# Kernel tuning notes

Hardware: AMD Instinct MI355X
Metric: run time of the kernel (lower is better)

Reference implementation:

```python
import jax, jax.numpy as jnp
import numpy as np

D_MODEL = 1024
N_HEAD = 16
DEPTH = D_MODEL // N_HEAD
NEG = -10000.0


def setup_inputs() -> dict:
    key = jax.random.key(0)
    ks = jax.random.split(key, 10)
    B, N = 4, 2048
    s = 1.0 / np.sqrt(D_MODEL)
    inp = {
        "input": jax.random.normal(ks[0], (B, N, D_MODEL), dtype=jnp.float32),
        "mask": jnp.tril(jnp.ones((N, N), dtype=bool)),  # causal; True = attend
        "Wq": jax.random.normal(ks[1], (D_MODEL, D_MODEL), dtype=jnp.float32) * s,
        "bq": jnp.zeros((D_MODEL,), dtype=jnp.float32),
        "Wk": jax.random.normal(ks[2], (D_MODEL, D_MODEL), dtype=jnp.float32) * s,
        "bk": jnp.zeros((D_MODEL,), dtype=jnp.float32),
        "Wv": jax.random.normal(ks[3], (D_MODEL, D_MODEL), dtype=jnp.float32) * s,
        "bv": jnp.zeros((D_MODEL,), dtype=jnp.float32),
        "Wo": jax.random.normal(ks[4], (D_MODEL, D_MODEL), dtype=jnp.float32) * s,
        "bo": jnp.zeros((D_MODEL,), dtype=jnp.float32),
    }
    return inp


def reference(input, mask, Wq, bq, Wk, bk, Wv, bv, Wo, bo):
    b, n, _ = input.shape
    # torch Linear: x @ W.T + b  (dropout is identity in eval)
    q = (input @ Wq.T + bq).reshape(b, n, N_HEAD, DEPTH)
    k = (input @ Wk.T + bk).reshape(b, n, N_HEAD, DEPTH)
    v = (input @ Wv.T + bv).reshape(b, n, N_HEAD, DEPTH)
    # per-head scale is sqrt(depth) (ScaledDotProductAttention built with d_model=depth)
    scale = jnp.sqrt(jnp.asarray(DEPTH, dtype=input.dtype))
    scores = jnp.einsum("bnhd,bmhd->bhnm", q, k) / scale
    scores = jnp.where(mask, scores, NEG)
    attn = jax.nn.softmax(scores, axis=-1)
    out = jnp.einsum("bhnm,bmhd->bnhd", attn, v).reshape(b, n, D_MODEL)
    return out @ Wo.T + bo
```

## Files before the change

### kernel.cpp

```cpp
#include <hip/hip_runtime.h>
#include <hip/hip_bf16.h>
#include <stdint.h>

#define D_MODEL 1024
#define N_HEAD  16
#define DEPTH   64
#define BATCH   4
#define SEQ     2048
#define ROWS    (BATCH*SEQ)
#define LOG2E   1.4426950408889634f
#define QSCALE  0.18033688292839513f

typedef unsigned short u16;
typedef __attribute__((ext_vector_type(8))) short short8;
typedef __attribute__((ext_vector_type(4))) float f32x4;

__device__ inline u16 f2bf(float f) {
  union { float f; unsigned u; } v; v.f = f;
  unsigned r = v.u + 0x7FFFu + ((v.u >> 16) & 1u);
  return (u16)(r >> 16);
}

__device__ inline unsigned cvt_pk_bf16(float lo, float hi) {
  unsigned w;
  asm("v_cvt_pk_bf16_f32 %0, %1, %2" : "=v"(w) : "v"(lo), "v"(hi));
  return w;
}

__device__ inline void gll16(const void* g, void* l) {
  __builtin_amdgcn_global_load_lds(
      (const __attribute__((address_space(1))) void*)g,
      (__attribute__((address_space(3))) void*)l, 16, 0, 0);
}

__global__ __launch_bounds__(256) void cvt_all(
    const float4* __restrict__ X,  const float4* __restrict__ Wq,
    const float4* __restrict__ Wk, const float4* __restrict__ Wv,
    const float4* __restrict__ Wo,
    u16* __restrict__ Xb, u16* __restrict__ Wqkvb, u16* __restrict__ Wob)
{
  const int b = blockIdx.x;
  const float4* src; u16* dst; int lb;
  if      (b < 8192)  { src = X;  dst = Xb;                        lb = b; }
  else if (b < 9216)  { src = Wq; dst = Wqkvb;                     lb = b - 8192; }
  else if (b < 10240) { src = Wk; dst = Wqkvb + D_MODEL*D_MODEL;   lb = b - 9216; }
  else if (b < 11264) { src = Wv; dst = Wqkvb + 2*D_MODEL*D_MODEL; lb = b - 10240; }
  else                { src = Wo; dst = Wob;                       lb = b - 11264; }
  const int i = lb*256 + threadIdx.x;
  float4 v = src[i];
  ushort4 o;
  o.x = f2bf(v.x); o.y = f2bf(v.y); o.z = f2bf(v.z); o.w = f2bf(v.w);
  *(ushort4*)(dst + 4*(size_t)i) = o;
}

__global__ __launch_bounds__(256) void gemm_qkv(
    const u16* __restrict__ A, const u16* __restrict__ Bm,
    const float* __restrict__ bq, const float* __restrict__ bk,
    const float* __restrict__ bvp,
    u16* __restrict__ Qo, u16* __restrict__ Ko, u16* __restrict__ Vo)
{
  constexpr int K = D_MODEL, BK = 64;
  __shared__ __align__(16) u16 As[128*BK];
  __shared__ __align__(16) u16 Bs[128*BK];
  const int tid = threadIdx.x;
  const int wave = tid >> 6, lane = tid & 63;
  const int g = lane >> 4, c = lane & 15;
  const int m0 = blockIdx.x * 128, n0 = blockIdx.y * 128;
  const int wr = (wave >> 1) * 64, wc = (wave & 1) * 64;
  f32x4 acc[4][4] = {};

  int aRow[4], aCol[4];
#pragma unroll
  for (int cc = 0; cc < 4; ++cc) {
    int L = (wave*4 + cc)*1024 + lane*16;
    int U = L ^ (((L >> 7) & 7) << 4);
    aRow[cc] = U >> 7;
    aCol[cc] = (U & 127) >> 1;
  }

  for (int k0 = 0; k0 < K; k0 += BK) {
#pragma unroll
    for (int cc = 0; cc < 4; ++cc) {
      int chunk = wave*4 + cc;
      gll16(A  + (size_t)(m0 + aRow[cc])*K + k0 + aCol[cc], (char*)As + chunk*1024);
      gll16(Bm + (size_t)(n0 + aRow[cc])*K + k0 + aCol[cc], (char*)Bs + chunk*1024);
    }
    __syncthreads();
#pragma unroll
    for (int ks = 0; ks < 2; ++ks) {
      short8 af[4], bf[4];
#pragma unroll
      for (int rb = 0; rb < 4; ++rb) {
        int row = wr + rb*16 + c;
        int addr = (row*128 + ks*64 + g*16) ^ ((row & 7) << 4);
        af[rb] = *(const short8*)((const char*)As + addr);
      }
#pragma unroll
      for (int cb = 0; cb < 4; ++cb) {
        int row = wc + cb*16 + c;
        int addr = (row*128 + ks*64 + g*16) ^ ((row & 7) << 4);
        bf[cb] = *(const short8*)((const char*)Bs + addr);
      }
#pragma unroll
      for (int rb = 0; rb < 4; ++rb)
#pragma unroll
        for (int cb = 0; cb < 4; ++cb)
          acc[rb][cb] = __builtin_amdgcn_mfma_f32_16x16x32_bf16(af[rb], bf[cb], acc[rb][cb], 0, 0, 0);
    }
    __syncthreads();
  }

  const int mode = n0 >> 10;
  const float* bias = (mode == 0) ? bq : (mode == 1) ? bk : bvp;

#pragma unroll
  for (int rb = 0; rb < 4; ++rb) {
#pragma unroll
    for (int cb = 0; cb < 4; ++cb) {
      int colg = n0 + wc + cb*16 + c;
      int cl = colg & 1023;
      int h = cl >> 6, d = cl & 63;
      float bv = bias[cl];
      if (mode == 2) {
        int rg = m0 + wr + rb*16 + g*4;
        int b = rg >> 11, n = rg & 2047;
        ushort4 o;
        o.x = f2bf(acc[rb][cb][0] + bv);
        o.y = f2bf(acc[rb][cb][1] + bv);
        o.z = f2bf(acc[rb][cb][2] + bv);
        o.w = f2bf(acc[rb][cb][3] + bv);
        *(ushort4*)&Vo[(((size_t)(b*N_HEAD + h))*DEPTH + d)*SEQ + n] = o;
      } else {
        u16* dst = (mode == 0) ? Qo : Ko;
        float sc = (mode == 0) ? QSCALE : 1.0f;
#pragma unroll
        for (int r = 0; r < 4; ++r) {
          int rowg = m0 + wr + rb*16 + g*4 + r;
          int b = rowg >> 11, n = rowg & 2047;
          dst[(((size_t)(b*N_HEAD + h))*SEQ + n)*DEPTH + d] = f2bf((acc[rb][cb][r] + bv) * sc);
        }
      }
    }
  }
}

__global__ __launch_bounds__(256) void gemm_out(
    const u16* __restrict__ A, const u16* __restrict__ Bm,
    const float* __restrict__ bias, float* __restrict__ Cout,
    int M, int N, int K)
{
  constexpr int BK = 64;
  __shared__ __align__(16) u16 As[128*BK];
  __shared__ __align__(16) u16 Bs[128*BK];
  const int tid = threadIdx.x;
  const int wave = tid >> 6, lane = tid & 63;
  const int g = lane >> 4, c = lane & 15;
  const int m0 = blockIdx.x * 128, n0 = blockIdx.y * 128;
  const int wr = (wave >> 1) * 64, wc = (wave & 1) * 64;
  f32x4 acc[4][4] = {};

  int aRow[4], aCol[4];
#pragma unroll
  for (int cc = 0; cc < 4; ++cc) {
    int L = (wave*4 + cc)*1024 + lane*16;
    int U = L ^ (((L >> 7) & 7) << 4);
    aRow[cc] = U >> 7;
    aCol[cc] = (U & 127) >> 1;
  }

  for (int k0 = 0; k0 < K; k0 += BK) {
#pragma unroll
    for (int cc = 0; cc < 4; ++cc) {
      int chunk = wave*4 + cc;
      gll16(A  + (size_t)(m0 + aRow[cc])*K + k0 + aCol[cc], (char*)As + chunk*1024);
      gll16(Bm + (size_t)(n0 + aRow[cc])*K + k0 + aCol[cc], (char*)Bs + chunk*1024);
    }
    __syncthreads();
#pragma unroll
    for (int ks = 0; ks < 2; ++ks) {
      short8 af[4], bf[4];
#pragma unroll
      for (int rb = 0; rb < 4; ++rb) {
        int row = wr + rb*16 + c;
        int addr = (row*128 + ks*64 + g*16) ^ ((row & 7) << 4);
        af[rb] = *(const short8*)((const char*)As + addr);
      }
#pragma unroll
      for (int cb = 0; cb < 4; ++cb) {
        int row = wc + cb*16 + c;
        int addr = (row*128 + ks*64 + g*16) ^ ((row & 7) << 4);
        bf[cb] = *(const short8*)((const char*)Bs + addr);
      }
#pragma unroll
      for (int rb = 0; rb < 4; ++rb)
#pragma unroll
        for (int cb = 0; cb < 4; ++cb)
          acc[rb][cb] = __builtin_amdgcn_mfma_f32_16x16x32_bf16(af[rb], bf[cb], acc[rb][cb], 0, 0, 0);
    }
    __syncthreads();
  }

#pragma unroll
  for (int rb = 0; rb < 4; ++rb) {
#pragma unroll
    for (int cb = 0; cb < 4; ++cb) {
      int colg = n0 + wc + cb*16 + c;
      float bv = bias[colg];
#pragma unroll
      for (int r = 0; r < 4; ++r) {
        int rowg = m0 + wr + rb*16 + g*4 + r;
        Cout[(size_t)rowg * N + colg] = acc[rb][cb][r] + bv;
      }
    }
  }
}

__global__ __launch_bounds__(512) void flash(
    const u16* __restrict__ Q, const u16* __restrict__ K,
    const u16* __restrict__ VT, u16* __restrict__ O)
{
  __shared__ __align__(16) u16 Ks[2][64*64];
  __shared__ __align__(16) u16 Vs[2][64*64];
  const int tid = threadIdx.x, wave = tid >> 6, lane = tid & 63;
  const int g = lane >> 4, c = lane & 15;
  const int bh = blockIdx.y, b = bh >> 4, h = bh & 15;
  const int qt = gridDim.x - 1 - blockIdx.x;
  const int q0 = qt * 128;
  const int qg = q0 + wave*16 + c;
  const u16* Qh = Q  + (size_t)bh * SEQ * DEPTH;
  const u16* Kh = K  + (size_t)bh * SEQ * DEPTH;
  const u16* Vh = VT + (size_t)bh * DEPTH * SEQ;

  short8 qf[2];
#pragma unroll
  for (int ks = 0; ks < 2; ++ks)
    qf[ks] = *(const short8*)(Qh + (size_t)(q0 + wave*16 + c)*DEPTH + ks*32 + g*8);

  f32x4 o[4] = {};
  float m_r = -3.0e38f, l_r = 0.0f;

  const int src1 = (c + (((2*g)  & 3) << 4)) << 2;
  const int src2 = (c + (((2*g+1)& 3) << 4)) << 2;
  const bool hi = (g >> 1) & 1;

  int sRow, sCol;
  {
    int L = wave*1024 + lane*16;
    int U = L ^ (((L >> 7) & 7) << 4);
    sRow = U >> 7; sCol = (U & 127) >> 1;
  }

  auto stage = [&](int t, int bsel) {
    const int kv0 = t * 64;
    gll16(Kh + (size_t)(kv0 + sRow)*DEPTH + sCol, (char*)Ks[bsel] + wave*1024);
    gll16(Vh + (size_t)sRow*SEQ + kv0 + sCol,     (char*)Vs[bsel] + wave*1024);
  };

  const int ntiles = 2*qt + 2;
  stage(0, 0);
  __syncthreads();
  int cur = 0;

  for (int t = 0; t < ntiles; ++t) {
    if (t + 1 < ntiles) stage(t + 1, cur ^ 1);
    const int kv0 = t * 64;

    if (kv0 <= q0 + wave*16 + 15) {
      const char* Kc = (const char*)Ks[cur];
      const char* Vc = (const char*)Vs[cur];

      f32x4 s[4] = {};
#pragma unroll
      for (int ks = 0; ks < 2; ++ks)
#pragma unroll
        for (int cb = 0; cb < 4; ++cb) {
          int row = cb*16 + c;
          int addr = (row*128 + ks*64 + g*16) ^ ((row & 7) << 4);
          short8 kf = *(const short8*)(Kc + addr);
          s[cb] = __builtin_amdgcn_mfma_f32_16x16x32_bf16(kf, qf[ks], s[cb], 0, 0, 0);
        }

      if (t >= ntiles - 2) {
#pragma unroll
        for (int cb = 0; cb < 4; ++cb)
#pragma unroll
          for (int r = 0; r < 4; ++r)
            if (kv0 + cb*16 + g*4 + r > qg) s[cb][r] = -3.0e38f;
      }

      float mx = s[0][0];
#pragma unroll
      for (int cb = 0; cb < 4; ++cb)
#pragma unroll
        for (int r = 0; r < 4; ++r) mx = fmaxf(mx, s[cb][r]);
      mx = fmaxf(mx, __shfl_xor(mx, 16));
      mx = fmaxf(mx, __shfl_xor(mx, 32));

      float mn = fmaxf(m_r, mx);
      float alpha = exp2f(m_r - mn);
      m_r = mn;

      float sum = 0.f;
      unsigned pk01[4], pk23[4];
#pragma unroll
      for (int cb = 0; cb < 4; ++cb) {
        float p0 = exp2f(s[cb][0] - mn);
        float p1 = exp2f(s[cb][1] - mn);
        float p2 = exp2f(s[cb][2] - mn);
        float p3 = exp2f(s[cb][3] - mn);
        sum += (p0 + p1) + (p2 + p3);
        pk01[cb] = cvt_pk_bf16(p0, p1);
        pk23[cb] = cvt_pk_bf16(p2, p3);
      }
      sum += __shfl_xor(sum, 16);
      sum += __shfl_xor(sum, 32);
      l_r = l_r*alpha + sum;
#pragma unroll
      for (int db = 0; db < 4; ++db)
#pragma unroll
        for (int r = 0; r < 4; ++r) o[db][r] *= alpha;

#pragma unroll
      for (int js = 0; js < 2; ++js) {
        unsigned a0  = __builtin_amdgcn_ds_bpermute(src1, pk01[2*js]);
        unsigned a0b = __builtin_amdgcn_ds_bpermute(src1, pk01[2*js+1]);
        unsigned a1  = __builtin_amdgcn_ds_bpermute(src1, pk23[2*js]);
        unsigned a1b = __builtin_amdgcn_ds_bpermute(src1, pk23[2*js+1]);
        unsigned b0  = __builtin_amdgcn_ds_bpermute(src2, pk01[2*js]);
        unsigned b0b = __builtin_amdgcn_ds_bpermute(src2, pk01[2*js+1]);
        unsigned b1  = __builtin_amdgcn_ds_bpermute(src2, pk23[2*js]);
        unsigned b1b = __builtin_amdgcn_ds_bpermute(src2, pk23[2*js+1]);
        union { unsigned u[4]; short8 v8; } pf;
        pf.u[0] = hi ? a0b : a0;
        pf.u[1] = hi ? a1b : a1;
        pf.u[2] = hi ? b0b : b0;
        pf.u[3] = hi ? b1b : b1;
#pragma unroll
        for (int db = 0; db < 4; ++db) {
          int row = db*16 + c;
          int addr = (row*128 + js*64 + g*16) ^ ((row & 7) << 4);
          short8 vf = *(const short8*)(Vc + addr);
          o[db] = __builtin_amdgcn_mfma_f32_16x16x32_bf16(vf, pf.v8, o[db], 0, 0, 0);
        }
      }
    }
    __syncthreads();
    cur ^= 1;
  }

  float inv = 1.0f / l_r;
  size_t base = ((size_t)(b*SEQ + qg))*D_MODEL + h*DEPTH;
#pragma unroll
  for (int db = 0; db < 4; ++db) {
    ushort4 w;
    w.x = f2bf(o[db][0] * inv);
    w.y = f2bf(o[db][1] * inv);
    w.z = f2bf(o[db][2] * inv);
    w.w = f2bf(o[db][3] * inv);
    *(ushort4*)&O[base + db*16 + g*4] = w;
  }
}

extern "C" void kernel_launch(void* const* d_in, const int* in_sizes, int n_in,
                              void* d_out, int out_size, void* d_ws, size_t ws_size,
                              hipStream_t stream) {
  const float* X  = (const float*)d_in[0];
  const float* Wq = (const float*)d_in[2];
  const float* bq = (const float*)d_in[3];
  const float* Wk = (const float*)d_in[4];
  const float* bk = (const float*)d_in[5];
  const float* Wv = (const float*)d_in[6];
  const float* bv = (const float*)d_in[7];
  const float* Wo = (const float*)d_in[8];
  const float* bo = (const float*)d_in[9];

  char* w = (char*)d_ws;
  const size_t MB = 1u << 20;
  u16* Xb   = (u16*)(w);
  u16* Qb   = (u16*)(w + 16*MB);
  u16* Kb   = (u16*)(w + 32*MB);
  u16* VTb  = (u16*)(w + 48*MB);
  u16* Ob   = (u16*)(w + 64*MB);
  u16* Wqkv = (u16*)(w + 80*MB);
  u16* Wob  = (u16*)(w + 86*MB);

  cvt_all<<<12288, 256, 0, stream>>>(
      (const float4*)X, (const float4*)Wq, (const float4*)Wk,
      (const float4*)Wv, (const float4*)Wo, Xb, Wqkv, Wob);

  gemm_qkv<<<dim3(ROWS/128, 3*D_MODEL/128), 256, 0, stream>>>(
      Xb, Wqkv, bq, bk, bv, Qb, Kb, VTb);

  flash<<<dim3(SEQ/128, BATCH*N_HEAD), 512, 0, stream>>>(Qb, Kb, VTb, Ob);

  gemm_out<<<dim3(ROWS/128, D_MODEL/128), 256, 0, stream>>>(
      Ob, Wob, bo, (float*)d_out, ROWS, D_MODEL, D_MODEL);
}
```

Measured before the change: 355.6 us.

## Shrink flash query tile to 64 rows with 1D heavy-first grid and setprio

The flash kernel now uses 64-query tiles with 4 waves per block instead of 128-query tiles with 8 waves. It launches a 1D grid of 2048 blocks ordered so the longest causal tiles start first, with each wave staging two chunks of the K/V loads. Every wave in a tile now has live work on every KV tile, so the per-wave causal skip branch is removed and masking happens only on the diagonal tile. s_setprio is raised around the MFMA sections to favour matrix issue. This aims to cut idle waves and improve load balance and occupancy, at the cost of reloading K/V twice as often per query row.

```diff
diff --git a/kernel.cpp b/kernel.cpp
--- a/kernel.cpp
+++ b/kernel.cpp
@@ -215,7 +215,7 @@
   }
 }
 
-__global__ __launch_bounds__(512) void flash(
+__global__ __launch_bounds__(256) void flash(
     const u16* __restrict__ Q, const u16* __restrict__ K,
     const u16* __restrict__ VT, u16* __restrict__ O)
 {
@@ -223,9 +223,10 @@
   __shared__ __align__(16) u16 Vs[2][64*64];
   const int tid = threadIdx.x, wave = tid >> 6, lane = tid & 63;
   const int g = lane >> 4, c = lane & 15;
-  const int bh = blockIdx.y, b = bh >> 4, h = bh & 15;
-  const int qt = gridDim.x - 1 - blockIdx.x;
-  const int q0 = qt * 128;
+  const int bid = blockIdx.x;
+  const int qt = 31 - (bid >> 6);
+  const int bh = bid & 63, b = bh >> 4, h = bh & 15;
+  const int q0 = qt * 64;
   const int qg = q0 + wave*16 + c;
   const u16* Qh = Q  + (size_t)bh * SEQ * DEPTH;
   const u16* Kh = K  + (size_t)bh * SEQ * DEPTH;
@@ -234,7 +235,7 @@
   short8 qf[2];
 #pragma unroll
   for (int ks = 0; ks < 2; ++ks)
-    qf[ks] = *(const short8*)(Qh + (size_t)(q0 + wave*16 + c)*DEPTH + ks*32 + g*8);
+    qf[ks] = *(const short8*)(Qh + (size_t)qg*DEPTH + ks*32 + g*8);
 
   f32x4 o[4] = {};
   float m_r = -3.0e38f, l_r = 0.0f;
@@ -243,20 +244,25 @@
   const int src2 = (c + (((2*g+1)& 3) << 4)) << 2;
   const bool hi = (g >> 1) & 1;
 
-  int sRow, sCol;
-  {
-    int L = wave*1024 + lane*16;
+  int sRow[2], sCol[2];
+#pragma unroll
+  for (int cc = 0; cc < 2; ++cc) {
+    int L = (wave*2 + cc)*1024 + lane*16;
     int U = L ^ (((L >> 7) & 7) << 4);
-    sRow = U >> 7; sCol = (U & 127) >> 1;
+    sRow[cc] = U >> 7; sCol[cc] = (U & 127) >> 1;
   }
 
   auto stage = [&](int t, int bsel) {
     const int kv0 = t * 64;
-    gll16(Kh + (size_t)(kv0 + sRow)*DEPTH + sCol, (char*)Ks[bsel] + wave*1024);
-    gll16(Vh + (size_t)sRow*SEQ + kv0 + sCol,     (char*)Vs[bsel] + wave*1024);
+#pragma unroll
+    for (int cc = 0; cc < 2; ++cc) {
+      int chunk = wave*2 + cc;
+      gll16(Kh + (size_t)(kv0 + sRow[cc])*DEPTH + sCol[cc], (char*)Ks[bsel] + chunk*1024);
+      gll16(Vh + (size_t)sRow[cc]*SEQ + kv0 + sCol[cc],     (char*)Vs[bsel] + chunk*1024);
+    }
   };
 
-  const int ntiles = 2*qt + 2;
+  const int ntiles = qt + 1;
   stage(0, 0);
   __syncthreads();
   int cur = 0;
@@ -264,85 +270,86 @@
   for (int t = 0; t < ntiles; ++t) {
     if (t + 1 < ntiles) stage(t + 1, cur ^ 1);
     const int kv0 = t * 64;
-
-    if (kv0 <= q0 + wave*16 + 15) {
-      const char* Kc = (const char*)Ks[cur];
-      const char* Vc = (const char*)Vs[cur];
-
-      f32x4 s[4] = {};
-#pragma unroll
-      for (int ks = 0; ks < 2; ++ks)
-#pragma unroll
-        for (int cb = 0; cb < 4; ++cb) {
-          int row = cb*16 + c;
-          int addr = (row*128 + ks*64 + g*16) ^ ((row & 7) << 4);
-          short8 kf = *(const short8*)(Kc + addr);
-          s[cb] = __builtin_amdgcn_mfma_f32_16x16x32_bf16(kf, qf[ks], s[cb], 0, 0, 0);
-        }
-
-      if (t >= ntiles - 2) {
-#pragma unroll
-        for (int cb = 0; cb < 4; ++cb)
-#pragma unroll
-          for (int r = 0; r < 4; ++r)
-            if (kv0 + cb*16 + g*4 + r > qg) s[cb][r] = -3.0e38f;
-      }
-
-      float mx = s[0][0];
+    const char* Kc = (const char*)Ks[cur];
+    const char* Vc = (const char*)Vs[cur];
+
+    f32x4 s[4] = {};
+    __builtin_amdgcn_s_setprio(1);
+#pragma unroll
+    for (int ks = 0; ks < 2; ++ks)
+#pragma unroll
+      for (int cb = 0; cb < 4; ++cb) {
+        int row = cb*16 + c;
+        int addr = (row*128 + ks*64 + g*16) ^ ((row & 7) << 4);
+        short8 kf = *(const short8*)(Kc + addr);
+        s[cb] = __builtin_amdgcn_mfma_f32_16x16x32_bf16(kf, qf[ks], s[cb], 0, 0, 0);
+      }
+    __builtin_amdgcn_s_setprio(0);
+
+    if (t == ntiles - 1) {
 #pragma unroll
       for (int cb = 0; cb < 4; ++cb)
 #pragma unroll
-        for (int r = 0; r < 4; ++r) mx = fmaxf(mx, s[cb][r]);
-      mx = fmaxf(mx, __shfl_xor(mx, 16));
-      mx = fmaxf(mx, __shfl_xor(mx, 32));
-
-      float mn = fmaxf(m_r, mx);
-      float alpha = exp2f(m_r - mn);
-      m_r = mn;
-
-      float sum = 0.f;
-      unsigned pk01[4], pk23[4];
-#pragma unroll
-      for (int cb = 0; cb < 4; ++cb) {
-        float p0 = exp2f(s[cb][0] - mn);
-        float p1 = exp2f(s[cb][1] - mn);
-        float p2 = exp2f(s[cb][2] - mn);
-        float p3 = exp2f(s[cb][3] - mn);
-        sum += (p0 + p1) + (p2 + p3);
-        pk01[cb] = cvt_pk_bf16(p0, p1);
-        pk23[cb] = cvt_pk_bf16(p2, p3);
-      }
-      sum += __shfl_xor(sum, 16);
-      sum += __shfl_xor(sum, 32);
-      l_r = l_r*alpha + sum;
-#pragma unroll
-      for (int db = 0; db < 4; ++db)
-#pragma unroll
-        for (int r = 0; r < 4; ++r) o[db][r] *= alpha;
-
-#pragma unroll
-      for (int js = 0; js < 2; ++js) {
-        unsigned a0  = __builtin_amdgcn_ds_bpermute(src1, pk01[2*js]);
-        unsigned a0b = __builtin_amdgcn_ds_bpermute(src1, pk01[2*js+1]);
-        unsigned a1  = __builtin_amdgcn_ds_bpermute(src1, pk23[2*js]);
-        unsigned a1b = __builtin_amdgcn_ds_bpermute(src1, pk23[2*js+1]);
-        unsigned b0  = __builtin_amdgcn_ds_bpermute(src2, pk01[2*js]);
-        unsigned b0b = __builtin_amdgcn_ds_bpermute(src2, pk01[2*js+1]);
-        unsigned b1  = __builtin_amdgcn_ds_bpermute(src2, pk23[2*js]);
-        unsigned b1b = __builtin_amdgcn_ds_bpermute(src2, pk23[2*js+1]);
-        union { unsigned u[4]; short8 v8; } pf;
-        pf.u[0] = hi ? a0b : a0;
-        pf.u[1] = hi ? a1b : a1;
-        pf.u[2] = hi ? b0b : b0;
-        pf.u[3] = hi ? b1b : b1;
-#pragma unroll
-        for (int db = 0; db < 4; ++db) {
-          int row = db*16 + c;
-          int addr = (row*128 + js*64 + g*16) ^ ((row & 7) << 4);
-          short8 vf = *(const short8*)(Vc + addr);
-          o[db] = __builtin_amdgcn_mfma_f32_16x16x32_bf16(vf, pf.v8, o[db], 0, 0, 0);
-        }
-      }
+        for (int r = 0; r < 4; ++r)
+          if (kv0 + cb*16 + g*4 + r > qg) s[cb][r] = -3.0e38f;
+    }
+
+    float mx = s[0][0];
+#pragma unroll
+    for (int cb = 0; cb < 4; ++cb)
+#pragma unroll
+      for (int r = 0; r < 4; ++r) mx = fmaxf(mx, s[cb][r]);
+    mx = fmaxf(mx, __shfl_xor(mx, 16));
+    mx = fmaxf(mx, __shfl_xor(mx, 32));
+
+    float mn = fmaxf(m_r, mx);
+    float alpha = exp2f(m_r - mn);
+    m_r = mn;
+
+    float sum = 0.f;
+    unsigned pk01[4], pk23[4];
+#pragma unroll
+    for (int cb = 0; cb < 4; ++cb) {
+      float p0 = exp2f(s[cb][0] - mn);
+      float p1 = exp2f(s[cb][1] - mn);
+      float p2 = exp2f(s[cb][2] - mn);
+      float p3 = exp2f(s[cb][3] - mn);
+      sum += (p0 + p1) + (p2 + p3);
+      pk01[cb] = cvt_pk_bf16(p0, p1);
+      pk23[cb] = cvt_pk_bf16(p2, p3);
+    }
+    sum += __shfl_xor(sum, 16);
+    sum += __shfl_xor(sum, 32);
+    l_r = l_r*alpha + sum;
+#pragma unroll
+    for (int db = 0; db < 4; ++db)
+#pragma unroll
+      for (int r = 0; r < 4; ++r) o[db][r] *= alpha;
+
+#pragma unroll
+    for (int js = 0; js < 2; ++js) {
+      unsigned a0  = __builtin_amdgcn_ds_bpermute(src1, pk01[2*js]);
+      unsigned a0b = __builtin_amdgcn_ds_bpermute(src1, pk01[2*js+1]);
+      unsigned a1  = __builtin_amdgcn_ds_bpermute(src1, pk23[2*js]);
+      unsigned a1b = __builtin_amdgcn_ds_bpermute(src1, pk23[2*js+1]);
+      unsigned b0  = __builtin_amdgcn_ds_bpermute(src2, pk01[2*js]);
+      unsigned b0b = __builtin_amdgcn_ds_bpermute(src2, pk01[2*js+1]);
+      unsigned b1  = __builtin_amdgcn_ds_bpermute(src2, pk23[2*js]);
+      unsigned b1b = __builtin_amdgcn_ds_bpermute(src2, pk23[2*js+1]);
+      union { unsigned u[4]; short8 v8; } pf;
+      pf.u[0] = hi ? a0b : a0;
+      pf.u[1] = hi ? a1b : a1;
+      pf.u[2] = hi ? b0b : b0;
+      pf.u[3] = hi ? b1b : b1;
+      __builtin_amdgcn_s_setprio(1);
+#pragma unroll
+      for (int db = 0; db < 4; ++db) {
+        int row = db*16 + c;
+        int addr = (row*128 + js*64 + g*16) ^ ((row & 7) << 4);
+        short8 vf = *(const short8*)(Vc + addr);
+        o[db] = __builtin_amdgcn_mfma_f32_16x16x32_bf16(vf, pf.v8, o[db], 0, 0, 0);
+      }
+      __builtin_amdgcn_s_setprio(0);
     }
     __syncthreads();
     cur ^= 1;
@@ -391,7 +398,7 @@
   gemm_qkv<<<dim3(ROWS/128, 3*D_MODEL/128), 256, 0, stream>>>(
       Xb, Wqkv, bq, bk, bv, Qb, Kb, VTb);
 
-  flash<<<dim3(SEQ/128, BATCH*N_HEAD), 512, 0, stream>>>(Qb, Kb, VTb, Ob);
+  flash<<<2048, 256, 0, stream>>>(Qb, Kb, VTb, Ob);
 
   gemm_out<<<dim3(ROWS/128, D_MODEL/128), 256, 0, stream>>>(
       Ob, Wob, bo, (float*)d_out, ROWS, D_MODEL, D_MODEL);
```

Result: faster. 293.2 us (-17.5%).
